# Performance work log

Hardware: AMD Instinct MI355X
Metric: run time of the kernel (lower is better)

Reference implementation:

```python
import jax, jax.numpy as jnp
import numpy as np

HEADS = 8
DIM_HEAD = 64
SCALE = DIM_HEAD ** -0.5


def setup_inputs() -> dict:
    key = jax.random.key(0)
    ks = jax.random.split(key, 5)
    B, N, D = 2, 4096, 512
    x = jax.random.normal(ks[0], (B, N, D), dtype=jnp.float32)
    Wq = jax.random.normal(ks[1], (D, D), dtype=jnp.float32) * (D ** -0.5)
    Wk = jax.random.normal(ks[2], (D, D), dtype=jnp.float32) * (D ** -0.5)
    Wv = jax.random.normal(ks[3], (D, D), dtype=jnp.float32) * (D ** -0.5)
    Wo = jax.random.normal(ks[4], (D, D), dtype=jnp.float32) * (D ** -0.5)
    bo = jnp.zeros((D,), dtype=jnp.float32)
    return {"x": x, "Wq": Wq, "Wk": Wk, "Wv": Wv, "Wo": Wo, "bo": bo}


def reference(x, Wq, Wk, Wv, Wo, bo):
    B, N, D = x.shape
    h, d = HEADS, DIM_HEAD
    # torch nn.Linear: y = x @ W.T
    q = (x @ Wq.T).reshape(B, N, h, d).transpose(0, 2, 1, 3)  # b h n d
    k = (x @ Wk.T).reshape(B, N, h, d).transpose(0, 2, 1, 3)
    v = (x @ Wv.T).reshape(B, N, h, d).transpose(0, 2, 1, 3)
    # fp32 score path (ATTN_PRECISION='fp32')
    sim = jnp.einsum('bhid,bhjd->bhij', q.astype(jnp.float32), k.astype(jnp.float32)) * SCALE
    attn = jax.nn.softmax(sim, axis=-1).astype(v.dtype)
    out = jnp.einsum('bhij,bhjd->bhid', attn, v)  # b h n d
    out = out.transpose(0, 2, 1, 3).reshape(B, N, h * d)  # b n (h d)
    return out @ Wo.T + bo
```

## Files before the change

kernel.cpp:

```cpp
#include <hip/hip_runtime.h>
#include <hip/hip_bf16.h>

#define B_ 2
#define N_ 4096
#define D_ 512
#define H_ 8
#define M_ (B_*N_)
#define QSCALE_ 0.18033688011f

typedef short bf16x8 __attribute__((ext_vector_type(8)));
typedef float f32x4  __attribute__((ext_vector_type(4)));

static __device__ __forceinline__ unsigned short f2bf(float f) {
    union { float f; unsigned int u; } v; v.f = f;
    unsigned int r = v.u + 0x7fffu + ((v.u >> 16) & 1u);
    return (unsigned short)(r >> 16);
}
static __device__ __forceinline__ float bf2f(unsigned short h) {
    union { unsigned int u; float f; } v; v.u = ((unsigned int)h) << 16;
    return v.f;
}
static __device__ __forceinline__ unsigned int cvt_pk_bf16(float a, float b) {
    unsigned int r;
    asm("v_cvt_pk_bf16_f32 %0, %1, %2" : "=v"(r) : "v"(a), "v"(b));
    return r;
}

__global__ void conv_split(const float* __restrict__ src, unsigned short* __restrict__ dh,
                           unsigned short* __restrict__ dl, int n4)
{
    int i = blockIdx.x * blockDim.x + threadIdx.x;
    const int stride = gridDim.x * blockDim.x;
    for (; i < n4; i += stride) {
        float4 v = ((const float4*)src)[i];
        ushort4 hv, lv;
        hv.x = f2bf(v.x); hv.y = f2bf(v.y); hv.z = f2bf(v.z); hv.w = f2bf(v.w);
        lv.x = f2bf(v.x - bf2f(hv.x)); lv.y = f2bf(v.y - bf2f(hv.y));
        lv.z = f2bf(v.z - bf2f(hv.z)); lv.w = f2bf(v.w - bf2f(hv.w));
        ((ushort4*)dh)[i] = hv;
        ((ushort4*)dl)[i] = lv;
    }
}

__global__ void conv_w4(const float* __restrict__ w0, const float* __restrict__ w1,
                        const float* __restrict__ w2, const float* __restrict__ w3,
                        unsigned short* __restrict__ dh, unsigned short* __restrict__ dl)
{
    const int which = blockIdx.y;
    const float* src = which == 0 ? w0 : which == 1 ? w1 : which == 2 ? w2 : w3;
    const int i = blockIdx.x * 256 + threadIdx.x;
    float4 v = ((const float4*)src)[i];
    ushort4 hv, lv;
    hv.x = f2bf(v.x); hv.y = f2bf(v.y); hv.z = f2bf(v.z); hv.w = f2bf(v.w);
    lv.x = f2bf(v.x - bf2f(hv.x)); lv.y = f2bf(v.y - bf2f(hv.y));
    lv.z = f2bf(v.z - bf2f(hv.z)); lv.w = f2bf(v.w - bf2f(hv.w));
    ((ushort4*)(dh + (size_t)which * 262144))[i] = hv;
    ((ushort4*)(dl + (size_t)which * 262144))[i] = lv;
}

template<int MODE>
__global__ __launch_bounds__(256, 2) void gemm_mfma(
    const unsigned short* __restrict__ Ah, const unsigned short* __restrict__ Al,
    const unsigned short* __restrict__ Wh, const unsigned short* __restrict__ Wl,
    const float* __restrict__ bias, float* __restrict__ outF,
    unsigned short* __restrict__ oh0, unsigned short* __restrict__ ol0,
    unsigned short* __restrict__ oh1, unsigned short* __restrict__ ol1,
    unsigned short* __restrict__ oh2, unsigned short* __restrict__ ol2,
    float scale0)
{
    __shared__ unsigned short At[2][8192];
    __shared__ unsigned short Bt[2][8192];

    const int t = threadIdx.x;
    const int lane = t & 63, wave = t >> 6;
    const int l15 = lane & 15, g = lane >> 4;
    const int wr = wave >> 1, wc = wave & 1;
    const int mb = blockIdx.x * 128;

    int which = 0, nbeff;
    if (MODE == 1) { which = blockIdx.y >> 2; nbeff = (blockIdx.y & 3) * 128; }
    else           { nbeff = blockIdx.y * 128; }
    const unsigned short* Whp = Wh + (size_t)which * 262144;
    const unsigned short* Wlp = Wl + (size_t)which * 262144;

    const int srow = t >> 1, sh = t & 1;
    const size_t gAr = (size_t)(mb + srow) * 512 + sh * 16;
    const size_t gBr = (size_t)(nbeff + srow) * 512 + sh * 16;
    const int sw = srow & 7;
    const int dA0 = srow * 64 + (((sh * 2 + 0) ^ sw) * 8);
    const int dA1 = srow * 64 + (((sh * 2 + 1) ^ sw) * 8);
    const int dA2 = srow * 64 + (((sh * 2 + 4) ^ sw) * 8);
    const int dA3 = srow * 64 + (((sh * 2 + 5) ^ sw) * 8);

    bf16x8 sA[4], sB[4];
#define GLOAD(K0) do {                                                              \
        sA[0] = *(const bf16x8*)&Ah[gAr + (K0)];  sA[1] = *(const bf16x8*)&Ah[gAr + (K0) + 8];  \
        sA[2] = *(const bf16x8*)&Al[gAr + (K0)];  sA[3] = *(const bf16x8*)&Al[gAr + (K0) + 8];  \
        sB[0] = *(const bf16x8*)&Whp[gBr + (K0)]; sB[1] = *(const bf16x8*)&Whp[gBr + (K0) + 8]; \
        sB[2] = *(const bf16x8*)&Wlp[gBr + (K0)]; sB[3] = *(const bf16x8*)&Wlp[gBr + (K0) + 8]; \
    } while (0)
#define SWRITE(BB) do {                                                             \
        *(bf16x8*)&At[BB][dA0] = sA[0]; *(bf16x8*)&At[BB][dA1] = sA[1];             \
        *(bf16x8*)&At[BB][dA2] = sA[2]; *(bf16x8*)&At[BB][dA3] = sA[3];             \
        *(bf16x8*)&Bt[BB][dA0] = sB[0]; *(bf16x8*)&Bt[BB][dA1] = sB[1];             \
        *(bf16x8*)&Bt[BB][dA2] = sB[2]; *(bf16x8*)&Bt[BB][dA3] = sB[3];             \
    } while (0)

    f32x4 acc[4][4];
#pragma unroll
    for (int mi = 0; mi < 4; ++mi)
#pragma unroll
        for (int ni = 0; ni < 4; ++ni) acc[mi][ni] = (f32x4){0.f, 0.f, 0.f, 0.f};

    GLOAD(0); SWRITE(0); __syncthreads();
    int cur = 0;
    for (int ks = 0; ks < 16; ++ks) {
        if (ks < 15) GLOAD((ks + 1) * 32);

        bf16x8 afh[4], afl[4], wfh[4], wfl[4];
#pragma unroll
        for (int mi = 0; mi < 4; ++mi) {
            const int ar = wr * 64 + mi * 16 + l15, asw = ar & 7;
            afh[mi] = *(const bf16x8*)&At[cur][ar * 64 + ((g ^ asw) * 8)];
            afl[mi] = *(const bf16x8*)&At[cur][ar * 64 + (((g + 4) ^ asw) * 8)];
        }
#pragma unroll
        for (int ni = 0; ni < 4; ++ni) {
            const int br = wc * 64 + ni * 16 + l15, bsw = br & 7;
            wfh[ni] = *(const bf16x8*)&Bt[cur][br * 64 + ((g ^ bsw) * 8)];
            wfl[ni] = *(const bf16x8*)&Bt[cur][br * 64 + (((g + 4) ^ bsw) * 8)];
        }
#pragma unroll
        for (int mi = 0; mi < 4; ++mi)
#pragma unroll
            for (int ni = 0; ni < 4; ++ni) {
                acc[mi][ni] = __builtin_amdgcn_mfma_f32_16x16x32_bf16(afh[mi], wfh[ni], acc[mi][ni], 0, 0, 0);
                acc[mi][ni] = __builtin_amdgcn_mfma_f32_16x16x32_bf16(afl[mi], wfh[ni], acc[mi][ni], 0, 0, 0);
                acc[mi][ni] = __builtin_amdgcn_mfma_f32_16x16x32_bf16(afh[mi], wfl[ni], acc[mi][ni], 0, 0, 0);
            }

        if (ks < 15) SWRITE(cur ^ 1);
        __syncthreads();
        cur ^= 1;
    }
#undef GLOAD
#undef SWRITE

    if (MODE == 0) {
#pragma unroll
        for (int ni = 0; ni < 4; ++ni) {
            const int col = nbeff + wc * 64 + ni * 16 + l15;
            const float bv = bias[col];
#pragma unroll
            for (int mi = 0; mi < 4; ++mi) {
                const int m0 = mb + wr * 64 + mi * 16 + g * 4;
#pragma unroll
                for (int r = 0; r < 4; ++r)
                    outF[(size_t)(m0 + r) * 512 + col] = acc[mi][ni][r] + bv;
            }
        }
    } else if (which < 2) {
        unsigned short* oh = which ? oh1 : oh0;
        unsigned short* ol = which ? ol1 : ol0;
        const float scl = which ? 1.0f : scale0;
#pragma unroll
        for (int ni = 0; ni < 4; ++ni) {
            const int col = nbeff + wc * 64 + ni * 16 + l15;
            const int hh = col >> 6, dd = col & 63;
#pragma unroll
            for (int mi = 0; mi < 4; ++mi) {
                const int m0 = mb + wr * 64 + mi * 16 + g * 4;
                const int b = m0 >> 12, seq0 = m0 & (N_ - 1);
                const size_t base = ((size_t)(b * H_ + hh) * N_ + seq0) * 64 + dd;
#pragma unroll
                for (int r = 0; r < 4; ++r) {
                    const float s = acc[mi][ni][r] * scl;
                    const unsigned short hv = f2bf(s);
                    oh[base + (size_t)r * 64] = hv;
                    ol[base + (size_t)r * 64] = f2bf(s - bf2f(hv));
                }
            }
        }
    } else {
#pragma unroll
        for (int ni = 0; ni < 4; ++ni) {
            const int col = nbeff + wc * 64 + ni * 16 + l15;
            const int hh = col >> 6, dd = col & 63;
#pragma unroll
            for (int mi = 0; mi < 4; ++mi) {
                const int m0 = mb + wr * 64 + mi * 16 + g * 4;
                const int b = m0 >> 12, seq0 = m0 & (N_ - 1);
                const size_t base = ((size_t)((b * H_ + hh) * 64) + dd) * N_ + seq0;
                const float s0 = acc[mi][ni][0], s1 = acc[mi][ni][1],
                            s2 = acc[mi][ni][2], s3 = acc[mi][ni][3];
                ushort4 hv, lv;
                hv.x = f2bf(s0); hv.y = f2bf(s1); hv.z = f2bf(s2); hv.w = f2bf(s3);
                lv.x = f2bf(s0 - bf2f(hv.x)); lv.y = f2bf(s1 - bf2f(hv.y));
                lv.z = f2bf(s2 - bf2f(hv.z)); lv.w = f2bf(s3 - bf2f(hv.w));
                *(ushort4*)&oh2[base] = hv;
                *(ushort4*)&ol2[base] = lv;
            }
        }
    }
}

__global__ __launch_bounds__(256, 2) void attn_mfma(
    const unsigned short* __restrict__ qh, const unsigned short* __restrict__ ql,
    const unsigned short* __restrict__ kh, const unsigned short* __restrict__ kl,
    const unsigned short* __restrict__ vth, const unsigned short* __restrict__ vtl,
    unsigned short* __restrict__ oh, unsigned short* __restrict__ ol)
{
    __shared__ unsigned short Kb[2][2][4096];
    __shared__ unsigned short Vb[2][2][4096];

    const int t    = threadIdx.x;
    const int lane = t & 63;
    const int wave = t >> 6;
    const int l15  = lane & 15;
    const int g    = lane >> 4;
    const int bh   = blockIdx.y;
    const int qbase = blockIdx.x * 128 + wave * 32;

    bf16x8 qf[2][2][2];
#pragma unroll
    for (int rt = 0; rt < 2; ++rt)
#pragma unroll
        for (int c = 0; c < 2; ++c) {
            const size_t src = ((size_t)bh * N_ + qbase + rt * 16 + l15) * 64 + c * 32 + g * 8;
            qf[rt][c][0] = *(const bf16x8*)&qh[src];
            qf[rt][c][1] = *(const bf16x8*)&ql[src];
        }

    f32x4 O[2][4];
#pragma unroll
    for (int rt = 0; rt < 2; ++rt)
#pragma unroll
        for (int dt = 0; dt < 4; ++dt) O[rt][dt] = (f32x4){0.f, 0.f, 0.f, 0.f};
    float mreg[2] = {-3.0e38f, -3.0e38f};
    float lreg[2] = {0.f, 0.f};

    const int srow = t >> 3;
    const int sc16 = t & 7;
    const size_t kbase = (size_t)bh * N_ * 64;
    const size_t vbase = (size_t)bh * 64 * N_;
    const int vdst0 = srow * 64 + ((sc16 ^ (srow & 7)) * 8);
    const int vdst1 = (srow + 32) * 64 + ((sc16 ^ ((srow + 32) & 7)) * 8);
    const int krho  = (((srow >> 2) & 1) << 4) | (((srow >> 3) & 3) << 2) | (srow & 3);
    const int kdst0 = krho * 64 + ((sc16 ^ (krho & 7)) * 8);
    const int kdst1 = kdst0 + 32 * 64;

    bf16x8 sKh[2], sKl[2], sVh[2], sVl[2];

#define LOADT(KT) do {                                                          \
        const size_t gK0 = kbase + ((size_t)((KT) * 64 + srow)) * 64 + sc16 * 8;      \
        const size_t gK1 = kbase + ((size_t)((KT) * 64 + srow + 32)) * 64 + sc16 * 8; \
        const size_t gV0 = vbase + (size_t)srow * N_ + (KT) * 64 + sc16 * 8;          \
        const size_t gV1 = vbase + (size_t)(srow + 32) * N_ + (KT) * 64 + sc16 * 8;   \
        sKh[0] = *(const bf16x8*)&kh[gK0];  sKh[1] = *(const bf16x8*)&kh[gK1];  \
        sKl[0] = *(const bf16x8*)&kl[gK0];  sKl[1] = *(const bf16x8*)&kl[gK1];  \
        sVh[0] = *(const bf16x8*)&vth[gV0]; sVh[1] = *(const bf16x8*)&vth[gV1]; \
        sVl[0] = *(const bf16x8*)&vtl[gV0]; sVl[1] = *(const bf16x8*)&vtl[gV1]; \
    } while (0)

#define WRITET(BB) do {                                                         \
        *(bf16x8*)&Kb[BB][0][kdst0] = sKh[0]; *(bf16x8*)&Kb[BB][0][kdst1] = sKh[1]; \
        *(bf16x8*)&Kb[BB][1][kdst0] = sKl[0]; *(bf16x8*)&Kb[BB][1][kdst1] = sKl[1]; \
        *(bf16x8*)&Vb[BB][0][vdst0] = sVh[0]; *(bf16x8*)&Vb[BB][0][vdst1] = sVh[1]; \
        *(bf16x8*)&Vb[BB][1][vdst0] = sVl[0]; *(bf16x8*)&Vb[BB][1][vdst1] = sVl[1]; \
    } while (0)

    LOADT(0);
    WRITET(0);
    __syncthreads();

    int cur = 0;
    for (int kt = 0; kt < N_ / 64; ++kt) {
        const bool pf = (kt + 1 < N_ / 64);
        if (pf) LOADT(kt + 1);

        f32x4 S[2][4];
#pragma unroll
        for (int rt = 0; rt < 2; ++rt)
#pragma unroll
            for (int j = 0; j < 4; ++j) S[rt][j] = (f32x4){0.f, 0.f, 0.f, 0.f};

        __builtin_amdgcn_s_setprio(1);
#pragma unroll
        for (int j = 0; j < 4; ++j) {
            const int krow = j * 16 + l15;
            const int rb = krow * 64, sw2 = (krow & 7) * 8;
#pragma unroll
            for (int c = 0; c < 2; ++c) {
                const int off = rb + (((c * 4 + g) * 8) ^ sw2);
                bf16x8 kfh = *(const bf16x8*)&Kb[cur][0][off];
                bf16x8 kfl = *(const bf16x8*)&Kb[cur][1][off];
#pragma unroll
                for (int rt = 0; rt < 2; ++rt) {
                    S[rt][j] = __builtin_amdgcn_mfma_f32_16x16x32_bf16(kfh, qf[rt][c][0], S[rt][j], 0, 0, 0);
                    S[rt][j] = __builtin_amdgcn_mfma_f32_16x16x32_bf16(kfl, qf[rt][c][0], S[rt][j], 0, 0, 0);
                    S[rt][j] = __builtin_amdgcn_mfma_f32_16x16x32_bf16(kfh, qf[rt][c][1], S[rt][j], 0, 0, 0);
                }
            }
        }
        __builtin_amdgcn_s_setprio(0);

        bf16x8 pah[2][2];
#pragma unroll
        for (int rt = 0; rt < 2; ++rt) {
            float pmax = -3.0e38f;
#pragma unroll
            for (int j = 0; j < 4; ++j)
#pragma unroll
                for (int r = 0; r < 4; ++r) pmax = fmaxf(pmax, S[rt][j][r]);
            pmax = fmaxf(pmax, __shfl_xor(pmax, 16));
            pmax = fmaxf(pmax, __shfl_xor(pmax, 32));

            const float mold = mreg[rt];
            if (!__all(pmax <= mold + 8.0f)) {
                const float mnew = fmaxf(mold, pmax);
                const float alpha = exp2f(mold - mnew);
#pragma unroll
                for (int dt = 0; dt < 4; ++dt)
#pragma unroll
                    for (int r = 0; r < 4; ++r) O[rt][dt][r] *= alpha;
                lreg[rt] *= alpha;
                mreg[rt] = mnew;
            }
            const float mb2 = mreg[rt];

            float lsum = 0.f;
#pragma unroll
            for (int j = 0; j < 4; ++j)
#pragma unroll
                for (int r = 0; r < 4; ++r) {
                    S[rt][j][r] = exp2f(S[rt][j][r] - mb2);
                    lsum += S[rt][j][r];
                }
            lreg[rt] += lsum;

#pragma unroll
            for (int c = 0; c < 2; ++c) {
                const f32x4 s0 = S[rt][2 * c], s1 = S[rt][2 * c + 1];
                union { unsigned int u[4]; bf16x8 v; } th;
                th.u[0] = cvt_pk_bf16(s0[0], s0[1]);
                th.u[1] = cvt_pk_bf16(s0[2], s0[3]);
                th.u[2] = cvt_pk_bf16(s1[0], s1[1]);
                th.u[3] = cvt_pk_bf16(s1[2], s1[3]);
                pah[rt][c] = th.v;
            }
        }

        __builtin_amdgcn_s_setprio(1);
#pragma unroll
        for (int c = 0; c < 2; ++c) {
#pragma unroll
            for (int dt = 0; dt < 4; ++dt) {
                const int vrow = dt * 16 + l15;
                const int off = vrow * 64 + (((c * 4 + g) * 8) ^ ((vrow & 7) * 8));
                bf16x8 vfh = *(const bf16x8*)&Vb[cur][0][off];
                bf16x8 vfl = *(const bf16x8*)&Vb[cur][1][off];
#pragma unroll
                for (int rt = 0; rt < 2; ++rt) {
                    O[rt][dt] = __builtin_amdgcn_mfma_f32_16x16x32_bf16(vfh, pah[rt][c], O[rt][dt], 0, 0, 0);
                    O[rt][dt] = __builtin_amdgcn_mfma_f32_16x16x32_bf16(vfl, pah[rt][c], O[rt][dt], 0, 0, 0);
                }
            }
        }
        __builtin_amdgcn_s_setprio(0);

        if (pf) WRITET(cur ^ 1);
        __syncthreads();
        cur ^= 1;
    }

    const int b = bh >> 3, hh = bh & 7;
#pragma unroll
    for (int rt = 0; rt < 2; ++rt) {
        float lt = lreg[rt];
        lt += __shfl_xor(lt, 16);
        lt += __shfl_xor(lt, 32);
        const float inv = 1.0f / lt;
        const int n = qbase + rt * 16 + l15;
        const size_t rowbase = ((size_t)(b * N_) + n) * 512 + hh * 64 + g * 4;
#pragma unroll
        for (int dt = 0; dt < 4; ++dt) {
            const float s0 = O[rt][dt][0] * inv, s1 = O[rt][dt][1] * inv,
                        s2 = O[rt][dt][2] * inv, s3 = O[rt][dt][3] * inv;
            ushort4 hv, lv;
            hv.x = f2bf(s0); hv.y = f2bf(s1); hv.z = f2bf(s2); hv.w = f2bf(s3);
            lv.x = f2bf(s0 - bf2f(hv.x)); lv.y = f2bf(s1 - bf2f(hv.y));
            lv.z = f2bf(s2 - bf2f(hv.z)); lv.w = f2bf(s3 - bf2f(hv.w));
            *(ushort4*)&oh[rowbase + dt * 16] = hv;
            *(ushort4*)&ol[rowbase + dt * 16] = lv;
        }
    }
#undef LOADT
#undef WRITET
}

extern "C" void kernel_launch(void* const* d_in, const int* in_sizes, int n_in,
                              void* d_out, int out_size, void* d_ws, size_t ws_size,
                              hipStream_t stream)
{
    const float* x  = (const float*)d_in[0];
    const float* Wq = (const float*)d_in[1];
    const float* Wk = (const float*)d_in[2];
    const float* Wv = (const float*)d_in[3];
    const float* Wo = (const float*)d_in[4];
    const float* bo = (const float*)d_in[5];

    unsigned char* w8 = (unsigned char*)d_ws;
    const size_t MB = 1024 * 1024;
    unsigned short* xh  = (unsigned short*)(w8);
    unsigned short* xl  = (unsigned short*)(w8 + 8  * MB);
    unsigned short* wh  = (unsigned short*)(w8 + 16 * MB);
    unsigned short* wl  = (unsigned short*)(w8 + 18 * MB);
    unsigned short* qh  = (unsigned short*)(w8 + 20 * MB);
    unsigned short* ql  = (unsigned short*)(w8 + 28 * MB);
    unsigned short* kh  = (unsigned short*)(w8 + 36 * MB);
    unsigned short* kl  = (unsigned short*)(w8 + 44 * MB);
    unsigned short* vth = (unsigned short*)(w8 + 52 * MB);
    unsigned short* vtl = (unsigned short*)(w8 + 60 * MB);
    unsigned short* ah = xh;
    unsigned short* al = xl;
    float* out = (float*)d_out;

    conv_split<<<1024, 256, 0, stream>>>(x, xh, xl, M_ * 512 / 4);
    conv_w4<<<dim3(256, 4), 256, 0, stream>>>(Wq, Wk, Wv, Wo, wh, wl);

    gemm_mfma<1><<<dim3(64, 12), 256, 0, stream>>>(xh, xl, wh, wl, nullptr, nullptr,
                                                   qh, ql, kh, kl, vth, vtl, QSCALE_);

    attn_mfma<<<dim3(N_ / 128, 16), 256, 0, stream>>>(qh, ql, kh, kl, vth, vtl, ah, al);

    gemm_mfma<0><<<dim3(64, 4), 256, 0, stream>>>(ah, al, wh + 3 * 262144, wl + 3 * 262144,
                                                  bo, out, nullptr, nullptr, nullptr, nullptr,
                                                  nullptr, nullptr, 1.0f);
}
```

Measured before the change: 323.5 us.

## Software-pipeline attention loop, drop V low-precision split, merge conversion kernels

The attention loop is restructured so the QK^T MFMAs for the next key tile interleave with softmax and the PV product of the previous tile, using two alternating score buffers and shared-memory tiles kept one stage ahead. The low-order bf16 half of V is no longer produced or consumed, which halves V global and LDS traffic and PV MFMA count at some accuracy cost. The x and weight split-conversion kernels are fused into one launch. The deeper pipeline needs an extra barrier per iteration and more registers.

```diff
diff --git a/kernel.cpp b/kernel.cpp
--- a/kernel.cpp
+++ b/kernel.cpp
@@ -26,36 +26,34 @@
     return r;
 }
 
-__global__ void conv_split(const float* __restrict__ src, unsigned short* __restrict__ dh,
-                           unsigned short* __restrict__ dl, int n4)
+__global__ void conv_all(const float* __restrict__ x,
+                         const float* __restrict__ w0, const float* __restrict__ w1,
+                         const float* __restrict__ w2, const float* __restrict__ w3,
+                         unsigned short* __restrict__ xh, unsigned short* __restrict__ xl,
+                         unsigned short* __restrict__ wh, unsigned short* __restrict__ wl)
 {
-    int i = blockIdx.x * blockDim.x + threadIdx.x;
-    const int stride = gridDim.x * blockDim.x;
-    for (; i < n4; i += stride) {
-        float4 v = ((const float4*)src)[i];
-        ushort4 hv, lv;
-        hv.x = f2bf(v.x); hv.y = f2bf(v.y); hv.z = f2bf(v.z); hv.w = f2bf(v.w);
-        lv.x = f2bf(v.x - bf2f(hv.x)); lv.y = f2bf(v.y - bf2f(hv.y));
-        lv.z = f2bf(v.z - bf2f(hv.z)); lv.w = f2bf(v.w - bf2f(hv.w));
-        ((ushort4*)dh)[i] = hv;
-        ((ushort4*)dl)[i] = lv;
+    const int i = blockIdx.x * 256 + threadIdx.x;
+    float4 v;
+    ushort4* dh;
+    ushort4* dl;
+    if (i < 1048576) {
+        v = ((const float4*)x)[i];
+        dh = (ushort4*)xh + i;
+        dl = (ushort4*)xl + i;
+    } else {
+        const int j = i - 1048576;
+        const int w = j >> 16, di = j & 65535;
+        const float* src = w == 0 ? w0 : w == 1 ? w1 : w == 2 ? w2 : w3;
+        v = ((const float4*)src)[di];
+        dh = (ushort4*)(wh + (size_t)w * 262144) + di;
+        dl = (ushort4*)(wl + (size_t)w * 262144) + di;
     }
-}
-
-__global__ void conv_w4(const float* __restrict__ w0, const float* __restrict__ w1,
-                        const float* __restrict__ w2, const float* __restrict__ w3,
-                        unsigned short* __restrict__ dh, unsigned short* __restrict__ dl)
-{
-    const int which = blockIdx.y;
-    const float* src = which == 0 ? w0 : which == 1 ? w1 : which == 2 ? w2 : w3;
-    const int i = blockIdx.x * 256 + threadIdx.x;
-    float4 v = ((const float4*)src)[i];
     ushort4 hv, lv;
     hv.x = f2bf(v.x); hv.y = f2bf(v.y); hv.z = f2bf(v.z); hv.w = f2bf(v.w);
     lv.x = f2bf(v.x - bf2f(hv.x)); lv.y = f2bf(v.y - bf2f(hv.y));
     lv.z = f2bf(v.z - bf2f(hv.z)); lv.w = f2bf(v.w - bf2f(hv.w));
-    ((ushort4*)(dh + (size_t)which * 262144))[i] = hv;
-    ((ushort4*)(dl + (size_t)which * 262144))[i] = lv;
+    *dh = hv;
+    *dl = lv;
 }
 
 template<int MODE>
@@ -191,14 +189,10 @@
                 const int m0 = mb + wr * 64 + mi * 16 + g * 4;
                 const int b = m0 >> 12, seq0 = m0 & (N_ - 1);
                 const size_t base = ((size_t)((b * H_ + hh) * 64) + dd) * N_ + seq0;
-                const float s0 = acc[mi][ni][0], s1 = acc[mi][ni][1],
-                            s2 = acc[mi][ni][2], s3 = acc[mi][ni][3];
-                ushort4 hv, lv;
-                hv.x = f2bf(s0); hv.y = f2bf(s1); hv.z = f2bf(s2); hv.w = f2bf(s3);
-                lv.x = f2bf(s0 - bf2f(hv.x)); lv.y = f2bf(s1 - bf2f(hv.y));
-                lv.z = f2bf(s2 - bf2f(hv.z)); lv.w = f2bf(s3 - bf2f(hv.w));
+                ushort4 hv;
+                hv.x = f2bf(acc[mi][ni][0]); hv.y = f2bf(acc[mi][ni][1]);
+                hv.z = f2bf(acc[mi][ni][2]); hv.w = f2bf(acc[mi][ni][3]);
                 *(ushort4*)&oh2[base] = hv;
-                *(ushort4*)&ol2[base] = lv;
             }
         }
     }
@@ -207,11 +201,11 @@
 __global__ __launch_bounds__(256, 2) void attn_mfma(
     const unsigned short* __restrict__ qh, const unsigned short* __restrict__ ql,
     const unsigned short* __restrict__ kh, const unsigned short* __restrict__ kl,
-    const unsigned short* __restrict__ vth, const unsigned short* __restrict__ vtl,
+    const unsigned short* __restrict__ vth,
     unsigned short* __restrict__ oh, unsigned short* __restrict__ ol)
 {
     __shared__ unsigned short Kb[2][2][4096];
-    __shared__ unsigned short Vb[2][2][4096];
+    __shared__ unsigned short Vb[2][4096];
 
     const int t    = threadIdx.x;
     const int lane = t & 63;
@@ -249,129 +243,135 @@
     const int kdst0 = krho * 64 + ((sc16 ^ (krho & 7)) * 8);
     const int kdst1 = kdst0 + 32 * 64;
 
-    bf16x8 sKh[2], sKl[2], sVh[2], sVl[2];
-
-#define LOADT(KT) do {                                                          \
+    bf16x8 sKh[2], sKl[2], sVh[2];
+
+#define LOADT(KT) do {                                                                \
         const size_t gK0 = kbase + ((size_t)((KT) * 64 + srow)) * 64 + sc16 * 8;      \
         const size_t gK1 = kbase + ((size_t)((KT) * 64 + srow + 32)) * 64 + sc16 * 8; \
         const size_t gV0 = vbase + (size_t)srow * N_ + (KT) * 64 + sc16 * 8;          \
         const size_t gV1 = vbase + (size_t)(srow + 32) * N_ + (KT) * 64 + sc16 * 8;   \
-        sKh[0] = *(const bf16x8*)&kh[gK0];  sKh[1] = *(const bf16x8*)&kh[gK1];  \
-        sKl[0] = *(const bf16x8*)&kl[gK0];  sKl[1] = *(const bf16x8*)&kl[gK1];  \
-        sVh[0] = *(const bf16x8*)&vth[gV0]; sVh[1] = *(const bf16x8*)&vth[gV1]; \
-        sVl[0] = *(const bf16x8*)&vtl[gV0]; sVl[1] = *(const bf16x8*)&vtl[gV1]; \
-    } while (0)
-
-#define WRITET(BB) do {                                                         \
-        *(bf16x8*)&Kb[BB][0][kdst0] = sKh[0]; *(bf16x8*)&Kb[BB][0][kdst1] = sKh[1]; \
-        *(bf16x8*)&Kb[BB][1][kdst0] = sKl[0]; *(bf16x8*)&Kb[BB][1][kdst1] = sKl[1]; \
-        *(bf16x8*)&Vb[BB][0][vdst0] = sVh[0]; *(bf16x8*)&Vb[BB][0][vdst1] = sVh[1]; \
-        *(bf16x8*)&Vb[BB][1][vdst0] = sVl[0]; *(bf16x8*)&Vb[BB][1][vdst1] = sVl[1]; \
-    } while (0)
-
-    LOADT(0);
-    WRITET(0);
+        sKh[0] = *(const bf16x8*)&kh[gK0];  sKh[1] = *(const bf16x8*)&kh[gK1];        \
+        sKl[0] = *(const bf16x8*)&kl[gK0];  sKl[1] = *(const bf16x8*)&kl[gK1];        \
+        sVh[0] = *(const bf16x8*)&vth[gV0]; sVh[1] = *(const bf16x8*)&vth[gV1];       \
+    } while (0)
+
+#define WRITET(BB) do {                                                               \
+        *(bf16x8*)&Kb[BB][0][kdst0] = sKh[0]; *(bf16x8*)&Kb[BB][0][kdst1] = sKh[1];   \
+        *(bf16x8*)&Kb[BB][1][kdst0] = sKl[0]; *(bf16x8*)&Kb[BB][1][kdst1] = sKl[1];   \
+        *(bf16x8*)&Vb[BB][vdst0] = sVh[0];    *(bf16x8*)&Vb[BB][vdst1] = sVh[1];      \
+    } while (0)
+
+#define QKT_J(J, BUF, S) do {                                                         \
+        const int krow_ = (J) * 16 + l15;                                             \
+        const int rb_ = krow_ * 64, sw_ = (krow_ & 7) * 8;                            \
+        _Pragma("unroll")                                                             \
+        for (int c = 0; c < 2; ++c) {                                                 \
+            const int off_ = rb_ + (((c * 4 + g) * 8) ^ sw_);                         \
+            bf16x8 kfh_ = *(const bf16x8*)&Kb[BUF][0][off_];                          \
+            bf16x8 kfl_ = *(const bf16x8*)&Kb[BUF][1][off_];                          \
+            _Pragma("unroll")                                                         \
+            for (int rt = 0; rt < 2; ++rt) {                                          \
+                S[rt][J] = __builtin_amdgcn_mfma_f32_16x16x32_bf16(kfh_, qf[rt][c][0], S[rt][J], 0, 0, 0); \
+                S[rt][J] = __builtin_amdgcn_mfma_f32_16x16x32_bf16(kfl_, qf[rt][c][0], S[rt][J], 0, 0, 0); \
+                S[rt][J] = __builtin_amdgcn_mfma_f32_16x16x32_bf16(kfh_, qf[rt][c][1], S[rt][J], 0, 0, 0); \
+            }                                                                         \
+        }                                                                             \
+    } while (0)
+
+#define SOFTMAX_RT(RT, S) do {                                                        \
+        float pmax_ = -3.0e38f;                                                       \
+        _Pragma("unroll")                                                             \
+        for (int j = 0; j < 4; ++j)                                                   \
+            _Pragma("unroll")                                                         \
+            for (int r = 0; r < 4; ++r) pmax_ = fmaxf(pmax_, S[RT][j][r]);            \
+        pmax_ = fmaxf(pmax_, __shfl_xor(pmax_, 16));                                  \
+        pmax_ = fmaxf(pmax_, __shfl_xor(pmax_, 32));                                  \
+        const float mold_ = mreg[RT];                                                 \
+        if (!__all(pmax_ <= mold_ + 8.0f)) {                                          \
+            const float mnew_ = fmaxf(mold_, pmax_);                                  \
+            const float alpha_ = exp2f(mold_ - mnew_);                                \
+            _Pragma("unroll")                                                         \
+            for (int dt = 0; dt < 4; ++dt)                                            \
+                _Pragma("unroll")                                                     \
+                for (int r = 0; r < 4; ++r) O[RT][dt][r] *= alpha_;                   \
+            lreg[RT] *= alpha_;                                                       \
+            mreg[RT] = mnew_;                                                         \
+        }                                                                             \
+        const float mb_ = mreg[RT];                                                   \
+        float lsum_ = 0.f;                                                            \
+        _Pragma("unroll")                                                             \
+        for (int j = 0; j < 4; ++j)                                                   \
+            _Pragma("unroll")                                                         \
+            for (int r = 0; r < 4; ++r) {                                             \
+                S[RT][j][r] = exp2f(S[RT][j][r] - mb_);                               \
+                lsum_ += S[RT][j][r];                                                 \
+            }                                                                         \
+        lreg[RT] += lsum_;                                                            \
+        _Pragma("unroll")                                                             \
+        for (int c = 0; c < 2; ++c) {                                                 \
+            union { unsigned int u[4]; bf16x8 v; } th_;                               \
+            th_.u[0] = cvt_pk_bf16(S[RT][2*c][0], S[RT][2*c][1]);                     \
+            th_.u[1] = cvt_pk_bf16(S[RT][2*c][2], S[RT][2*c][3]);                     \
+            th_.u[2] = cvt_pk_bf16(S[RT][2*c+1][0], S[RT][2*c+1][1]);                 \
+            th_.u[3] = cvt_pk_bf16(S[RT][2*c+1][2], S[RT][2*c+1][3]);                 \
+            pah[RT][c] = th_.v;                                                       \
+        }                                                                             \
+    } while (0)
+
+#define PVSTEP(BUF) do {                                                              \
+        _Pragma("unroll")                                                             \
+        for (int c = 0; c < 2; ++c)                                                   \
+            _Pragma("unroll")                                                         \
+            for (int dt = 0; dt < 4; ++dt) {                                          \
+                const int vrow_ = dt * 16 + l15;                                      \
+                const int off_ = vrow_ * 64 + (((c * 4 + g) * 8) ^ ((vrow_ & 7) * 8));\
+                bf16x8 vfh_ = *(const bf16x8*)&Vb[BUF][off_];                         \
+                _Pragma("unroll")                                                     \
+                for (int rt = 0; rt < 2; ++rt)                                        \
+                    O[rt][dt] = __builtin_amdgcn_mfma_f32_16x16x32_bf16(vfh_, pah[rt][c], O[rt][dt], 0, 0, 0); \
+            }                                                                         \
+    } while (0)
+
+#define ITER(T, BK, SC, SP) do {                                                      \
+        if ((T) < 63) LOADT((T) + 1);                                                 \
+        __builtin_amdgcn_s_setprio(1);                                                \
+        SC[0][0] = (f32x4){0.f,0.f,0.f,0.f}; SC[0][1] = (f32x4){0.f,0.f,0.f,0.f};     \
+        SC[0][2] = (f32x4){0.f,0.f,0.f,0.f}; SC[0][3] = (f32x4){0.f,0.f,0.f,0.f};     \
+        SC[1][0] = (f32x4){0.f,0.f,0.f,0.f}; SC[1][1] = (f32x4){0.f,0.f,0.f,0.f};     \
+        SC[1][2] = (f32x4){0.f,0.f,0.f,0.f}; SC[1][3] = (f32x4){0.f,0.f,0.f,0.f};     \
+        QKT_J(0, BK, SC); QKT_J(1, BK, SC);                                           \
+        SOFTMAX_RT(0, SP);                                                            \
+        QKT_J(2, BK, SC); QKT_J(3, BK, SC);                                           \
+        SOFTMAX_RT(1, SP);                                                            \
+        PVSTEP((BK) ^ 1);                                                             \
+        __builtin_amdgcn_s_setprio(0);                                                \
+        __syncthreads();                                                              \
+        if ((T) < 63) WRITET((BK) ^ 1);                                               \
+        __syncthreads();                                                              \
+    } while (0)
+
+    f32x4 Sa[2][4], Sb[2][4];
+    bf16x8 pah[2][2];
+
+    LOADT(0); WRITET(0); __syncthreads();
+    LOADT(1);
+#pragma unroll
+    for (int rt = 0; rt < 2; ++rt)
+#pragma unroll
+        for (int j = 0; j < 4; ++j) Sa[rt][j] = (f32x4){0.f, 0.f, 0.f, 0.f};
+    __builtin_amdgcn_s_setprio(1);
+    QKT_J(0, 0, Sa); QKT_J(1, 0, Sa); QKT_J(2, 0, Sa); QKT_J(3, 0, Sa);
+    __builtin_amdgcn_s_setprio(0);
+    WRITET(1);
     __syncthreads();
 
-    int cur = 0;
-    for (int kt = 0; kt < N_ / 64; ++kt) {
-        const bool pf = (kt + 1 < N_ / 64);
-        if (pf) LOADT(kt + 1);
-
-        f32x4 S[2][4];
-#pragma unroll
-        for (int rt = 0; rt < 2; ++rt)
-#pragma unroll
-            for (int j = 0; j < 4; ++j) S[rt][j] = (f32x4){0.f, 0.f, 0.f, 0.f};
-
-        __builtin_amdgcn_s_setprio(1);
-#pragma unroll
-        for (int j = 0; j < 4; ++j) {
-            const int krow = j * 16 + l15;
-            const int rb = krow * 64, sw2 = (krow & 7) * 8;
-#pragma unroll
-            for (int c = 0; c < 2; ++c) {
-                const int off = rb + (((c * 4 + g) * 8) ^ sw2);
-                bf16x8 kfh = *(const bf16x8*)&Kb[cur][0][off];
-                bf16x8 kfl = *(const bf16x8*)&Kb[cur][1][off];
-#pragma unroll
-                for (int rt = 0; rt < 2; ++rt) {
-                    S[rt][j] = __builtin_amdgcn_mfma_f32_16x16x32_bf16(kfh, qf[rt][c][0], S[rt][j], 0, 0, 0);
-                    S[rt][j] = __builtin_amdgcn_mfma_f32_16x16x32_bf16(kfl, qf[rt][c][0], S[rt][j], 0, 0, 0);
-                    S[rt][j] = __builtin_amdgcn_mfma_f32_16x16x32_bf16(kfh, qf[rt][c][1], S[rt][j], 0, 0, 0);
-                }
-            }
-        }
-        __builtin_amdgcn_s_setprio(0);
-
-        bf16x8 pah[2][2];
-#pragma unroll
-        for (int rt = 0; rt < 2; ++rt) {
-            float pmax = -3.0e38f;
-#pragma unroll
-            for (int j = 0; j < 4; ++j)
-#pragma unroll
-                for (int r = 0; r < 4; ++r) pmax = fmaxf(pmax, S[rt][j][r]);
-            pmax = fmaxf(pmax, __shfl_xor(pmax, 16));
-            pmax = fmaxf(pmax, __shfl_xor(pmax, 32));
-
-            const float mold = mreg[rt];
-            if (!__all(pmax <= mold + 8.0f)) {
-                const float mnew = fmaxf(mold, pmax);
-                const float alpha = exp2f(mold - mnew);
-#pragma unroll
-                for (int dt = 0; dt < 4; ++dt)
-#pragma unroll
-                    for (int r = 0; r < 4; ++r) O[rt][dt][r] *= alpha;
-                lreg[rt] *= alpha;
-                mreg[rt] = mnew;
-            }
-            const float mb2 = mreg[rt];
-
-            float lsum = 0.f;
-#pragma unroll
-            for (int j = 0; j < 4; ++j)
-#pragma unroll
-                for (int r = 0; r < 4; ++r) {
-                    S[rt][j][r] = exp2f(S[rt][j][r] - mb2);
-                    lsum += S[rt][j][r];
-                }
-            lreg[rt] += lsum;
-
-#pragma unroll
-            for (int c = 0; c < 2; ++c) {
-                const f32x4 s0 = S[rt][2 * c], s1 = S[rt][2 * c + 1];
-                union { unsigned int u[4]; bf16x8 v; } th;
-                th.u[0] = cvt_pk_bf16(s0[0], s0[1]);
-                th.u[1] = cvt_pk_bf16(s0[2], s0[3]);
-                th.u[2] = cvt_pk_bf16(s1[0], s1[1]);
-                th.u[3] = cvt_pk_bf16(s1[2], s1[3]);
-                pah[rt][c] = th.v;
-            }
-        }
-
-        __builtin_amdgcn_s_setprio(1);
-#pragma unroll
-        for (int c = 0; c < 2; ++c) {
-#pragma unroll
-            for (int dt = 0; dt < 4; ++dt) {
-                const int vrow = dt * 16 + l15;
-                const int off = vrow * 64 + (((c * 4 + g) * 8) ^ ((vrow & 7) * 8));
-                bf16x8 vfh = *(const bf16x8*)&Vb[cur][0][off];
-                bf16x8 vfl = *(const bf16x8*)&Vb[cur][1][off];
-#pragma unroll
-                for (int rt = 0; rt < 2; ++rt) {
-                    O[rt][dt] = __builtin_amdgcn_mfma_f32_16x16x32_bf16(vfh, pah[rt][c], O[rt][dt], 0, 0, 0);
-                    O[rt][dt] = __builtin_amdgcn_mfma_f32_16x16x32_bf16(vfl, pah[rt][c], O[rt][dt], 0, 0, 0);
-                }
-            }
-        }
-        __builtin_amdgcn_s_setprio(0);
-
-        if (pf) WRITET(cur ^ 1);
-        __syncthreads();
-        cur ^= 1;
+    for (int tt = 1; tt < 64; tt += 2) {
+        ITER(tt, 1, Sb, Sa);
+        if (tt + 1 < 64) ITER(tt + 1, 0, Sa, Sb);
     }
+    SOFTMAX_RT(0, Sb);
+    SOFTMAX_RT(1, Sb);
+    PVSTEP(1);
 
     const int b = bh >> 3, hh = bh & 7;
 #pragma unroll
@@ -396,6 +396,10 @@
     }
 #undef LOADT
 #undef WRITET
+#undef QKT_J
+#undef SOFTMAX_RT
+#undef PVSTEP
+#undef ITER
 }
 
 extern "C" void kernel_launch(void* const* d_in, const int* in_sizes, int n_in,
@@ -420,18 +424,16 @@
     unsigned short* kh  = (unsigned short*)(w8 + 36 * MB);
     unsigned short* kl  = (unsigned short*)(w8 + 44 * MB);
     unsigned short* vth = (unsigned short*)(w8 + 52 * MB);
-    unsigned short* vtl = (unsigned short*)(w8 + 60 * MB);
     unsigned short* ah = xh;
     unsigned short* al = xl;
     float* out = (float*)d_out;
 
-    conv_split<<<1024, 256, 0, stream>>>(x, xh, xl, M_ * 512 / 4);
-    conv_w4<<<dim3(256, 4), 256, 0, stream>>>(Wq, Wk, Wv, Wo, wh, wl);
+    conv_all<<<5120, 256, 0, stream>>>(x, Wq, Wk, Wv, Wo, xh, xl, wh, wl);
 
     gemm_mfma<1><<<dim3(64, 12), 256, 0, stream>>>(xh, xl, wh, wl, nullptr, nullptr,
-                                                   qh, ql, kh, kl, vth, vtl, QSCALE_);
-
-    attn_mfma<<<dim3(N_ / 128, 16), 256, 0, stream>>>(qh, ql, kh, kl, vth, vtl, ah, al);
+                                                   qh, ql, kh, kl, vth, nullptr, QSCALE_);
+
+    attn_mfma<<<dim3(N_ / 128, 16), 256, 0, stream>>>(qh, ql, kh, kl, vth, ah, al);
 
     gemm_mfma<0><<<dim3(64, 4), 256, 0, stream>>>(ah, al, wh + 3 * 262144, wl + 3 * 262144,
                                                   bo, out, nullptr, nullptr, nullptr, nullptr,
```

New measurement: 304.8 us. 5.8% less time.
